# Performance work log

Measured on AMD Instinct MI355X. Metric: run time of the kernel, lower is better.

The kernel has to match this reference:

```python
import jax, jax.numpy as jnp
import numpy as np

B, S, D, H = 2, 2048, 1024, 16
DK = D // H


def setup_inputs() -> dict:
    key = jax.random.key(0)
    ks = jax.random.split(key, 12)
    sc = 1.0 / np.sqrt(D)
    inp = {
        "q": jax.random.normal(ks[0], (B, S, D), jnp.float32),
        "k": jax.random.normal(ks[1], (B, S, D), jnp.float32),
        "v": jax.random.normal(ks[2], (B, S, D), jnp.float32),
        # causal mask, broadcastable over batch and heads
        "mask": jnp.tril(jnp.ones((S, S), jnp.int32))[None, None],
        "Wq": jax.random.normal(ks[3], (D, D), jnp.float32) * sc,
        "bq": jax.random.normal(ks[4], (D,), jnp.float32) * 0.02,
        "Wk": jax.random.normal(ks[5], (D, D), jnp.float32) * sc,
        "bk": jax.random.normal(ks[6], (D,), jnp.float32) * 0.02,
        "Wv": jax.random.normal(ks[7], (D, D), jnp.float32) * sc,
        "bv": jax.random.normal(ks[8], (D,), jnp.float32) * 0.02,
        "Wo": jax.random.normal(ks[9], (D, D), jnp.float32) * sc,
        "bo": jax.random.normal(ks[10], (D,), jnp.float32) * 0.02,
    }
    return inp


def reference(q, k, v, mask, Wq, bq, Wk, bk, Wv, bv, Wo, bo):
    b, s, _ = q.shape
    # QKV projections (torch Linear: x @ W.T + b)
    qh = (q @ Wq.T + bq).reshape(b, s, H, DK).transpose(0, 2, 1, 3)  # [B,H,S,DK]
    kh = (k @ Wk.T + bk).reshape(b, -1, H, DK).transpose(0, 2, 1, 3)
    vh = (v @ Wv.T + bv).reshape(b, -1, H, DK).transpose(0, 2, 1, 3)
    scores = jnp.einsum("bhqd,bhkd->bhqk", qh, kh) / np.sqrt(DK)  # [B,H,S,S]
    scores = jnp.where(mask == 0, jnp.float32(-1e9), scores)
    attn = jax.nn.softmax(scores, axis=-1)
    # dropout p=0.0 (eval) -> identity
    x = jnp.einsum("bhqk,bhkd->bhqd", attn, vh)  # [B,H,S,DK]
    x = x.transpose(0, 2, 1, 3).reshape(b, s, H * DK)
    return x @ Wo.T + bo
```

## Files before the change

kernel.cpp:

```cpp
#include <hip/hip_runtime.h>
#include <hip/hip_bf16.h>
#include <cstdint>
#include <cstddef>

using u16   = unsigned short;
using u32   = uint32_t;
using u16x4 = __attribute__((ext_vector_type(4))) unsigned short;
using u16x8 = __attribute__((ext_vector_type(8))) unsigned short;
using s16x8 = __attribute__((ext_vector_type(8))) short;
using f32x4 = __attribute__((ext_vector_type(4))) float;
using f32x16 = __attribute__((ext_vector_type(16))) float;

#define B_DIM  2
#define S_DIM  2048
#define D_DIM  1024
#define H_DIM  16
#define DK_DIM 64

__device__ __forceinline__ u16 f2bf(float f) {
  union { float f; uint32_t u; } c; c.f = f;
  uint32_t u = c.u;
  return (u16)((u + 0x7FFFu + ((u >> 16) & 1u)) >> 16);
}
__device__ __forceinline__ float bf2f(u16 v) {
  union { uint32_t u; float f; } c; c.u = (uint32_t)v << 16;
  return c.f;
}

__device__ __forceinline__ void gload16(const void* g, void* l) {
  __builtin_amdgcn_global_load_lds(
      (const __attribute__((address_space(1))) void*)g,
      (__attribute__((address_space(3))) void*)l, 16, 0, 0);
}

__device__ __forceinline__ int chunk_base(int qt) {
  return (qt < 4) ? qt
       : (qt < 8) ? 4 + 2 * (qt - 4)
       : (qt < 12) ? 12 + 3 * (qt - 8)
       : 24 + 4 * (qt - 12);
}

__global__ __launch_bounds__(256) void cast_all_kernel(
    const float* q, const float* k, const float* v,
    const float* wq, const float* wk, const float* wv, const float* wo,
    u16* dq, u16* dk, u16* dv, u16* dwq, u16* dwk, u16* dwv, u16* dwo)
{
  const int f = blockIdx.x;
  const float* s; u16* d; int base;
  if (f < 6144) {
    int a = f >> 11;
    s = (a == 0) ? q : (a == 1) ? k : v;
    d = (a == 0) ? dq : (a == 1) ? dk : dv;
    base = (f & 2047) * 2048;
  } else {
    int a = (f - 6144) >> 9;
    s = (a == 0) ? wq : (a == 1) ? wk : (a == 2) ? wv : wo;
    d = (a == 0) ? dwq : (a == 1) ? dwk : (a == 2) ? dwv : dwo;
    base = ((f - 6144) & 511) * 2048;
  }
  int i = base + threadIdx.x * 8;
  f32x4 a = *(const f32x4*)(s + i);
  f32x4 b = *(const f32x4*)(s + i + 4);
  u16x8 ov;
  ov[0] = f2bf(a[0]); ov[1] = f2bf(a[1]); ov[2] = f2bf(a[2]); ov[3] = f2bf(a[3]);
  ov[4] = f2bf(b[0]); ov[5] = f2bf(b[1]); ov[6] = f2bf(b[2]); ov[7] = f2bf(b[3]);
  *(u16x8*)(d + i) = ov;
}

#define BM 128
#define BK 64

template <int BNT>
__device__ __forceinline__ void gemm_bt_core(
    const u16* __restrict__ A, const u16* __restrict__ W,
    const float* __restrict__ bias, void* __restrict__ out, int mode,
    int mtile, int ntile, float oscale)
{
  constexpr int NFRAG = BNT / 32;
  __shared__ u16 Alds[BM * BK];
  __shared__ u16 Blds[BNT * BK];
  const int K = 1024;
  const int tid = threadIdx.x;
  const int w = tid >> 6, l = tid & 63;
  const int lr = l & 15, lg = l >> 4;
  const int wr = w >> 1, wc = w & 1;
  const int m0 = mtile * BM, n0 = ntile * BNT;

  f32x4 acc[4][NFRAG] = {};

  for (int kt = 0; kt < K / BK; ++kt) {
    const int k0 = kt * BK;
    #pragma unroll
    for (int i = 0; i < 4; ++i) {
      int c = i * 256 + tid;
      int r = c >> 3;
      int cb = ((c & 7) << 4) ^ ((r & 7) << 4);
      gload16((const char*)(A + (size_t)(m0 + r) * K + k0) + cb,
              (char*)Alds + i * 4096 + w * 1024);
    }
    #pragma unroll
    for (int i = 0; i < BNT / 32; ++i) {
      int c = i * 256 + tid;
      int r = c >> 3;
      int cb = ((c & 7) << 4) ^ ((r & 7) << 4);
      gload16((const char*)(W + (size_t)(n0 + r) * K + k0) + cb,
              (char*)Blds + i * 4096 + w * 1024);
    }
    __syncthreads();
    #pragma unroll
    for (int ks = 0; ks < 2; ++ks) {
      s16x8 af[4], bf[NFRAG];
      #pragma unroll
      for (int mi = 0; mi < 4; ++mi) {
        int r = wr * 64 + mi * 16 + lr;
        int kb = (ks * 64 + lg * 16) ^ ((r & 7) << 4);
        af[mi] = *(const s16x8*)((const char*)Alds + r * 128 + kb);
      }
      #pragma unroll
      for (int ni = 0; ni < NFRAG; ++ni) {
        int r = wc * (BNT / 2) + ni * 16 + lr;
        int kb = (ks * 64 + lg * 16) ^ ((r & 7) << 4);
        bf[ni] = *(const s16x8*)((const char*)Blds + r * 128 + kb);
      }
      #pragma unroll
      for (int mi = 0; mi < 4; ++mi)
        #pragma unroll
        for (int ni = 0; ni < NFRAG; ++ni)
          acc[mi][ni] = __builtin_amdgcn_mfma_f32_16x16x32_bf16(
              af[mi], bf[ni], acc[mi][ni], 0, 0, 0);
    }
    __syncthreads();
  }

  const int mbase = m0 + wr * 64 + lg * 4;
  const int nbase = n0 + wc * (BNT / 2) + lr;
  #pragma unroll
  for (int ni = 0; ni < NFRAG; ++ni) {
    int n = nbase + ni * 16;
    float bb = bias[n];
    #pragma unroll
    for (int mi = 0; mi < 4; ++mi) {
      int mr = mbase + mi * 16;
      f32x4 vv = acc[mi][ni];
      if (mode == 2) {
        float* o = (float*)out;
        #pragma unroll
        for (int r = 0; r < 4; ++r) o[(size_t)(mr + r) * 1024 + n] = vv[r] + bb;
      } else if (mode == 0) {
        u16* o = (u16*)out;
        #pragma unroll
        for (int r = 0; r < 4; ++r)
          o[(size_t)(mr + r) * 1024 + n] = f2bf((vv[r] + bb) * oscale);
      } else if (mode == 3) {
        u16* o = (u16*)out;
        int h = n >> 6, d = n & 63;
        int db = d >> 4, hi8 = (d >> 3) & 1, e = d & 7;
        int bb_ = mr >> 11, j = mr & (S_DIM - 1);
        int jt = j >> 6, rh = (j >> 5) & 1, lq0 = j & 31;
        size_t base = (((size_t)(bb_ * H_DIM + h) * 32 + jt) * 8 + (db * 2 + rh))
                      * 512 + (size_t)(hi8 * 32) * 8 + e;
        #pragma unroll
        for (int r = 0; r < 4; ++r)
          o[base + (size_t)(lq0 + r) * 8] = f2bf(vv[r] + bb);
      } else {
        u16* o = (u16*)out;
        int h = n >> 6, dk = n & 63;
        int rh = dk >> 5, lq = dk & 31;
        int bb_ = mr >> 11, j = mr & (S_DIM - 1);
        int jt = j >> 6, jj = j & 63;
        int db = jj >> 4, hi8 = (jj >> 3) & 1, e0 = jj & 7;
        size_t base = (((size_t)(bb_ * H_DIM + h) * 32 + jt) * 8 + (db * 2 + rh))
                      * 512 + (size_t)(hi8 * 32 + lq) * 8 + e0;
        u16x4 pk;
        #pragma unroll
        for (int r = 0; r < 4; ++r) pk[r] = f2bf(vv[r] + bb);
        *(u16x4*)(o + base) = pk;
      }
    }
  }
}

__global__ __launch_bounds__(256, 5) void qkv_gemm_kernel(
    const u16* xq, const u16* xk, const u16* xv,
    const u16* wq, const u16* wk, const u16* wv,
    const float* bq, const float* bk, const float* bv,
    u16* qlin, u16* kfragb, u16* vfragb)
{
  const int f = blockIdx.x;
  const int xcd = f & 7;
  const int s = f >> 3;
  const int z = s >> 6;
  const int r = s & 63;
  const int mtile = xcd * 4 + (r >> 4);
  const int ntile = r & 15;

  const u16* A = (z == 0) ? xq : (z == 1) ? xk : xv;
  const u16* W = (z == 0) ? wq : (z == 1) ? wk : wv;
  const float* bias = (z == 0) ? bq : (z == 1) ? bk : bv;
  void* out = (z == 0) ? (void*)qlin : (z == 1) ? (void*)kfragb : (void*)vfragb;
  gemm_bt_core<64>(A, W, bias, out, (z == 0) ? 0 : (z == 1) ? 3 : 1, mtile, ntile,
                   (z == 0) ? 0.125f * 1.44269504f : 1.0f);
}

__global__ __launch_bounds__(256, 5) void oproj_kernel(
    const u16* aout, const u16* wo, const float* bo, float* out)
{
  const int f = blockIdx.x;
  const int xcd = f & 7;
  const int s = f >> 3;
  const int mtile = xcd * 4 + (s >> 5);
  const int ntile = s & 31;
  gemm_bt_core<32>(aout, wo, bo, (void*)out, 2, mtile, ntile, 1.0f);
}

__global__ __launch_bounds__(256, 3) void attn_kernel(
    const u16* __restrict__ qlin, const u16* __restrict__ kfrag,
    const u16* __restrict__ vfrag, u16* __restrict__ opart,
    float* __restrict__ lpart)
{
  const int tid = threadIdx.x;
  const int w = tid >> 6, l = tid & 63;
  const int lq = l & 31, hi = l >> 5;

  const int f = blockIdx.x;
  const int bh = f & 31;
  const int g = f >> 5;
  int qt, ch;
  if (g < 16)      { qt = 15 - (g >> 2);        ch = g & 3; }
  else if (g < 28) { qt = 11 - (g - 16) / 3;    ch = (g - 16) % 3; }
  else if (g < 36) { qt = 7 - ((g - 28) >> 1);  ch = (g - 28) & 1; }
  else             { qt = 3 - (g - 36);         ch = 0; }
  const int T  = 2 * qt + 2;
  const int nc = (T + 7) >> 3;
  const int jlo = (ch * T) / nc;
  const int jhi = ((ch + 1) * T) / nc;
  const int b = bh >> 4, h = bh & 15;

  const int qb  = qt * 128 + w * 32;
  const int myq = qb + lq;
  const int jtend_w = (qb + 31) >> 6;
  const int jend = (jhi < jtend_w + 1) ? jhi : (jtend_w + 1);

  s16x8 qf[4];
  {
    const u16* qptr = qlin + (size_t)(b * S_DIM + myq) * D_DIM + h * DK_DIM + hi * 8;
    #pragma unroll
    for (int db = 0; db < 4; ++db) qf[db] = *(const s16x8*)(qptr + db * 16);
  }

  f32x16 o0 = {}, o1 = {};
  float l_run = 0.f;

  const u16* kbase = kfrag + (size_t)bh * 32 * 4096;
  const u16* vbase = vfrag + (size_t)bh * 32 * 4096;

  s16x8 kf2[8], vf2[8];
  #pragma unroll
  for (int fk = 0; fk < 8; ++fk)
    kf2[fk] = *(const s16x8*)(kbase + (size_t)jlo * 4096 + fk * 512 + (size_t)l * 8);
  #pragma unroll
  for (int fk = 0; fk < 8; ++fk)
    vf2[fk] = *(const s16x8*)(vbase + (size_t)jlo * 4096 + fk * 512 + (size_t)l * 8);

  #pragma unroll 1
  for (int jt = jlo; jt < jend; ++jt) {
    const int j0 = jt * 64;

    f32x16 s0 = {}, s1 = {};
    #pragma unroll
    for (int db = 0; db < 4; ++db) {
      s0 = __builtin_amdgcn_mfma_f32_32x32x16_bf16(kf2[db * 2 + 0], qf[db], s0, 0, 0, 0);
      s1 = __builtin_amdgcn_mfma_f32_32x32x16_bf16(kf2[db * 2 + 1], qf[db], s1, 0, 0, 0);
    }

    if (jt + 1 < jend) {
      const u16* kbn = kbase + (size_t)(jt + 1) * 4096;
      #pragma unroll
      for (int fk = 0; fk < 8; ++fk)
        kf2[fk] = *(const s16x8*)(kbn + fk * 512 + (size_t)l * 8);
    }

    if (j0 + 63 > qb) {
      #pragma unroll
      for (int r = 0; r < 16; ++r) {
        int kr = (r & 3) + 8 * (r >> 2) + 4 * hi;
        if (j0 + kr > myq)      s0[r] = -1e30f;
        if (j0 + 32 + kr > myq) s1[r] = -1e30f;
      }
    }

    u32 wds[16];
    float ls = 0.f;
    #pragma unroll
    for (int i = 0; i < 8; ++i) {
      float pa = __builtin_amdgcn_exp2f(s0[2 * i]);
      float pb = __builtin_amdgcn_exp2f(s0[2 * i + 1]);
      ls += pa + pb;
      wds[i] = (u32)f2bf(pa) | ((u32)f2bf(pb) << 16);
      float pc = __builtin_amdgcn_exp2f(s1[2 * i]);
      float pd = __builtin_amdgcn_exp2f(s1[2 * i + 1]);
      ls += pc + pd;
      wds[8 + i] = (u32)f2bf(pc) | ((u32)f2bf(pd) << 16);
    }
    l_run += ls;

    #pragma unroll
    for (int ks = 0; ks < 4; ++ks) {
      u32 w0 = wds[4 * ks], w1 = wds[4 * ks + 1];
      u32 w2 = wds[4 * ks + 2], w3 = wds[4 * ks + 3];
      u32 ta = __shfl_xor(hi ? w0 : w2, 32);
      u32 tb = __shfl_xor(hi ? w1 : w3, 32);
      union { u32 u[4]; s16x8 v; } pf;
      pf.u[0] = hi ? ta : w0;
      pf.u[1] = hi ? tb : w1;
      pf.u[2] = hi ? w2 : ta;
      pf.u[3] = hi ? w3 : tb;
      o0 = __builtin_amdgcn_mfma_f32_32x32x16_bf16(vf2[ks * 2 + 0], pf.v, o0, 0, 0, 0);
      o1 = __builtin_amdgcn_mfma_f32_32x32x16_bf16(vf2[ks * 2 + 1], pf.v, o1, 0, 0, 0);
    }

    if (jt + 1 < jend) {
      const u16* vbn = vbase + (size_t)(jt + 1) * 4096;
      #pragma unroll
      for (int fk = 0; fk < 8; ++fk)
        vf2[fk] = *(const s16x8*)(vbn + fk * 512 + (size_t)l * 8);
    }
  }

  const size_t gslot = (size_t)bh * 40 + chunk_base(qt) + ch;
  u16* ob = opart + ((gslot * 128) + w * 32 + lq) * 64;
  #pragma unroll
  for (int rq = 0; rq < 4; ++rq) {
    u16x4 pk0, pk1;
    #pragma unroll
    for (int j = 0; j < 4; ++j) {
      pk0[j] = f2bf(o0[rq * 4 + j]);
      pk1[j] = f2bf(o1[rq * 4 + j]);
    }
    *(u16x4*)(ob + rq * 8 + hi * 4)      = pk0;
    *(u16x4*)(ob + 32 + rq * 8 + hi * 4) = pk1;
  }
  float lt = l_run + __shfl_xor(l_run, 32);
  if (hi == 0) lpart[gslot * 128 + w * 32 + lq] = lt;
}

__global__ __launch_bounds__(256) void attn_combine_kernel(
    const u16* __restrict__ opart, const float* __restrict__ lpart,
    u16* __restrict__ aout)
{
  const int f = blockIdx.x;
  const int bh = f & 31, qt = f >> 5;
  const int b = bh >> 4, h = bh & 15;
  const int nc = (2 * qt + 9) >> 3;
  const int cs = chunk_base(qt);

  const int t = threadIdx.x;
  const int row = t >> 1, dbase = (t & 1) * 32;
  float acc[32] = {};
  float lsum = 0.f;
  for (int c = 0; c < nc; ++c) {
    const size_t slot = (size_t)bh * 40 + cs + c;
    const u16* pr = opart + ((slot * 128) + row) * 64 + dbase;
    #pragma unroll
    for (int v4 = 0; v4 < 4; ++v4) {
      u16x8 vv = *(const u16x8*)(pr + v4 * 8);
      #pragma unroll
      for (int j = 0; j < 8; ++j) acc[v4 * 8 + j] += bf2f(vv[j]);
    }
    lsum += lpart[slot * 128 + row];
  }
  float inv = 1.f / lsum;
  u16* orow = aout + ((size_t)b * S_DIM + qt * 128 + row) * D_DIM + h * 64 + dbase;
  #pragma unroll
  for (int v4 = 0; v4 < 4; ++v4) {
    u16x8 ov;
    #pragma unroll
    for (int j = 0; j < 8; ++j) ov[j] = f2bf(acc[v4 * 8 + j] * inv);
    *(u16x8*)(orow + v4 * 8) = ov;
  }
}

extern "C" void kernel_launch(void* const* d_in, const int* in_sizes, int n_in,
                              void* d_out, int out_size, void* d_ws, size_t ws_size,
                              hipStream_t stream)
{
  (void)in_sizes; (void)n_in; (void)out_size; (void)ws_size;
  const float* q  = (const float*)d_in[0];
  const float* k  = (const float*)d_in[1];
  const float* v  = (const float*)d_in[2];
  const float* Wq = (const float*)d_in[4];
  const float* bq = (const float*)d_in[5];
  const float* Wk = (const float*)d_in[6];
  const float* bk = (const float*)d_in[7];
  const float* Wv = (const float*)d_in[8];
  const float* bv = (const float*)d_in[9];
  const float* Wo = (const float*)d_in[10];
  const float* bo = (const float*)d_in[11];
  float* out = (float*)d_out;

  const size_t XSZ = (size_t)B_DIM * S_DIM * D_DIM;
  const size_t WSZ = (size_t)D_DIM * D_DIM;

  u16* p = (u16*)d_ws;
  u16* qbf  = p; p += XSZ;
  u16* kbf  = p; p += XSZ;
  u16* vbf  = p; p += XSZ;
  u16* wqb  = p; p += WSZ;
  u16* wkb  = p; p += WSZ;
  u16* wvb  = p; p += WSZ;
  u16* wob  = p; p += WSZ;
  u16* qlin   = p; p += XSZ;
  u16* kfragb = p; p += XSZ;
  u16* vfragb = p; p += XSZ;
  u16* aoutb  = p; p += XSZ;

  u16*   opart = (u16*)d_ws;
  float* lpart = (float*)((char*)d_ws + (size_t)1280 * 128 * 64 * 2);

  cast_all_kernel<<<8192, 256, 0, stream>>>(
      q, k, v, Wq, Wk, Wv, Wo, qbf, kbf, vbf, wqb, wkb, wvb, wob);
  qkv_gemm_kernel<<<1536, 256, 0, stream>>>(
      qbf, kbf, vbf, wqb, wkb, wvb, bq, bk, bv, qlin, kfragb, vfragb);
  attn_kernel<<<1280, 256, 0, stream>>>(qlin, kfragb, vfragb, opart, lpart);
  attn_combine_kernel<<<512, 256, 0, stream>>>(opart, lpart, aoutb);
  oproj_kernel<<<1024, 256, 0, stream>>>(aoutb, wob, bo, out);
}
```

Measured before the change: 120.3 us.

## Use 256x256 double-buffered tiles in the QKV projection GEMM

The QKV GEMM changes from 128x64 tiles with 256 threads to 256x256 tiles with 512 threads, and shared-memory staging is double-buffered so the next K-slice loads while the current one computes. The goal is more data reuse per block and less barrier stall. The shared template is split apart, so the output projection now has its own specialized copy with the same tile sizes as before. The trade-off is only 192 blocks on the GPU, fewer than the CU count, so some CUs sit idle. Each block also uses much more LDS (128 KB) and more accumulator registers.

```diff
diff --git a/kernel.cpp b/kernel.cpp
--- a/kernel.cpp
+++ b/kernel.cpp
@@ -67,86 +67,103 @@
   *(u16x8*)(d + i) = ov;
 }
 
-#define BM 128
-#define BK 64
-
-template <int BNT>
-__device__ __forceinline__ void gemm_bt_core(
-    const u16* __restrict__ A, const u16* __restrict__ W,
-    const float* __restrict__ bias, void* __restrict__ out, int mode,
-    int mtile, int ntile, float oscale)
-{
-  constexpr int NFRAG = BNT / 32;
-  __shared__ u16 Alds[BM * BK];
-  __shared__ u16 Blds[BNT * BK];
+__global__ __launch_bounds__(512, 2) void qkv_gemm_kernel(
+    const u16* xq, const u16* xk, const u16* xv,
+    const u16* wq, const u16* wk, const u16* wv,
+    const float* bq, const float* bk, const float* bv,
+    u16* qlin, u16* kfragb, u16* vfragb)
+{
+  __shared__ u16 Alds[2][256 * 64];
+  __shared__ u16 Blds[2][256 * 64];
+  const int f = blockIdx.x;
+  const int xcd = f & 7;
+  const int s = f >> 3;
+  const int z = s >> 3;
+  const int r8 = s & 7;
+  const int mtile = xcd * 2 + (r8 >> 2);
+  const int ntile = r8 & 3;
+
+  const u16* A = (z == 0) ? xq : (z == 1) ? xk : xv;
+  const u16* W = (z == 0) ? wq : (z == 1) ? wk : wv;
+  const float* bias = (z == 0) ? bq : (z == 1) ? bk : bv;
+  void* out = (z == 0) ? (void*)qlin : (z == 1) ? (void*)kfragb : (void*)vfragb;
+  const int mode = (z == 0) ? 0 : (z == 1) ? 3 : 1;
+  const float oscale = (z == 0) ? 0.125f * 1.44269504f : 1.0f;
+
   const int K = 1024;
   const int tid = threadIdx.x;
   const int w = tid >> 6, l = tid & 63;
   const int lr = l & 15, lg = l >> 4;
-  const int wr = w >> 1, wc = w & 1;
-  const int m0 = mtile * BM, n0 = ntile * BNT;
-
-  f32x4 acc[4][NFRAG] = {};
-
-  for (int kt = 0; kt < K / BK; ++kt) {
-    const int k0 = kt * BK;
+  const int wm = w >> 2, wn = w & 3;
+  const int m0 = mtile * 256, n0 = ntile * 256;
+
+  f32x4 acc[8][4] = {};
+
+  auto stage = [&](int buf, int kt) {
+    const int k0 = kt * 64;
     #pragma unroll
     for (int i = 0; i < 4; ++i) {
-      int c = i * 256 + tid;
+      int c = i * 512 + tid;
       int r = c >> 3;
       int cb = ((c & 7) << 4) ^ ((r & 7) << 4);
       gload16((const char*)(A + (size_t)(m0 + r) * K + k0) + cb,
-              (char*)Alds + i * 4096 + w * 1024);
-    }
-    #pragma unroll
-    for (int i = 0; i < BNT / 32; ++i) {
-      int c = i * 256 + tid;
+              (char*)&Alds[buf][0] + i * 8192 + w * 1024);
+    }
+    #pragma unroll
+    for (int i = 0; i < 4; ++i) {
+      int c = i * 512 + tid;
       int r = c >> 3;
       int cb = ((c & 7) << 4) ^ ((r & 7) << 4);
       gload16((const char*)(W + (size_t)(n0 + r) * K + k0) + cb,
-              (char*)Blds + i * 4096 + w * 1024);
-    }
-    __syncthreads();
+              (char*)&Blds[buf][0] + i * 8192 + w * 1024);
+    }
+  };
+
+  stage(0, 0);
+
+  #pragma unroll 1
+  for (int kt = 0; kt < 16; ++kt) {
+    const int cur = kt & 1;
+    asm volatile("s_waitcnt vmcnt(0)" ::: "memory");
+    __builtin_amdgcn_s_barrier();
+    __builtin_amdgcn_sched_barrier(0);
+    if (kt + 1 < 16) stage(cur ^ 1, kt + 1);
+
     #pragma unroll
     for (int ks = 0; ks < 2; ++ks) {
-      s16x8 af[4], bf[NFRAG];
-      #pragma unroll
-      for (int mi = 0; mi < 4; ++mi) {
-        int r = wr * 64 + mi * 16 + lr;
+      s16x8 af[8], bf[4];
+      #pragma unroll
+      for (int mi = 0; mi < 8; ++mi) {
+        int r = wm * 128 + mi * 16 + lr;
         int kb = (ks * 64 + lg * 16) ^ ((r & 7) << 4);
-        af[mi] = *(const s16x8*)((const char*)Alds + r * 128 + kb);
-      }
-      #pragma unroll
-      for (int ni = 0; ni < NFRAG; ++ni) {
-        int r = wc * (BNT / 2) + ni * 16 + lr;
+        af[mi] = *(const s16x8*)((const char*)&Alds[cur][0] + r * 128 + kb);
+      }
+      #pragma unroll
+      for (int ni = 0; ni < 4; ++ni) {
+        int r = wn * 64 + ni * 16 + lr;
         int kb = (ks * 64 + lg * 16) ^ ((r & 7) << 4);
-        bf[ni] = *(const s16x8*)((const char*)Blds + r * 128 + kb);
-      }
-      #pragma unroll
-      for (int mi = 0; mi < 4; ++mi)
+        bf[ni] = *(const s16x8*)((const char*)&Blds[cur][0] + r * 128 + kb);
+      }
+      #pragma unroll
+      for (int mi = 0; mi < 8; ++mi)
         #pragma unroll
-        for (int ni = 0; ni < NFRAG; ++ni)
+        for (int ni = 0; ni < 4; ++ni)
           acc[mi][ni] = __builtin_amdgcn_mfma_f32_16x16x32_bf16(
               af[mi], bf[ni], acc[mi][ni], 0, 0, 0);
     }
-    __syncthreads();
-  }
-
-  const int mbase = m0 + wr * 64 + lg * 4;
-  const int nbase = n0 + wc * (BNT / 2) + lr;
+  }
+
+  const int mbase = m0 + wm * 128 + lg * 4;
+  const int nbase = n0 + wn * 64 + lr;
   #pragma unroll
-  for (int ni = 0; ni < NFRAG; ++ni) {
+  for (int ni = 0; ni < 4; ++ni) {
     int n = nbase + ni * 16;
     float bb = bias[n];
     #pragma unroll
-    for (int mi = 0; mi < 4; ++mi) {
+    for (int mi = 0; mi < 8; ++mi) {
       int mr = mbase + mi * 16;
       f32x4 vv = acc[mi][ni];
-      if (mode == 2) {
-        float* o = (float*)out;
-        #pragma unroll
-        for (int r = 0; r < 4; ++r) o[(size_t)(mr + r) * 1024 + n] = vv[r] + bb;
-      } else if (mode == 0) {
+      if (mode == 0) {
         u16* o = (u16*)out;
         #pragma unroll
         for (int r = 0; r < 4; ++r)
@@ -180,37 +197,84 @@
   }
 }
 
-__global__ __launch_bounds__(256, 5) void qkv_gemm_kernel(
-    const u16* xq, const u16* xk, const u16* xv,
-    const u16* wq, const u16* wk, const u16* wv,
-    const float* bq, const float* bk, const float* bv,
-    u16* qlin, u16* kfragb, u16* vfragb)
-{
-  const int f = blockIdx.x;
-  const int xcd = f & 7;
-  const int s = f >> 3;
-  const int z = s >> 6;
-  const int r = s & 63;
-  const int mtile = xcd * 4 + (r >> 4);
-  const int ntile = r & 15;
-
-  const u16* A = (z == 0) ? xq : (z == 1) ? xk : xv;
-  const u16* W = (z == 0) ? wq : (z == 1) ? wk : wv;
-  const float* bias = (z == 0) ? bq : (z == 1) ? bk : bv;
-  void* out = (z == 0) ? (void*)qlin : (z == 1) ? (void*)kfragb : (void*)vfragb;
-  gemm_bt_core<64>(A, W, bias, out, (z == 0) ? 0 : (z == 1) ? 3 : 1, mtile, ntile,
-                   (z == 0) ? 0.125f * 1.44269504f : 1.0f);
-}
+#define BM 128
+#define BK 64
 
 __global__ __launch_bounds__(256, 5) void oproj_kernel(
-    const u16* aout, const u16* wo, const float* bo, float* out)
-{
+    const u16* __restrict__ aout, const u16* __restrict__ wo,
+    const float* __restrict__ bo, float* __restrict__ out)
+{
+  constexpr int BNT = 32;
+  __shared__ u16 Alds[BM * BK];
+  __shared__ u16 Blds[BNT * BK];
   const int f = blockIdx.x;
   const int xcd = f & 7;
   const int s = f >> 3;
   const int mtile = xcd * 4 + (s >> 5);
   const int ntile = s & 31;
-  gemm_bt_core<32>(aout, wo, bo, (void*)out, 2, mtile, ntile, 1.0f);
+
+  const int K = 1024;
+  const int tid = threadIdx.x;
+  const int w = tid >> 6, l = tid & 63;
+  const int lr = l & 15, lg = l >> 4;
+  const int wr = w >> 1, wc = w & 1;
+  const int m0 = mtile * BM, n0 = ntile * BNT;
+
+  f32x4 acc[4][1] = {};
+
+  for (int kt = 0; kt < K / BK; ++kt) {
+    const int k0 = kt * BK;
+    #pragma unroll
+    for (int i = 0; i < 4; ++i) {
+      int c = i * 256 + tid;
+      int r = c >> 3;
+      int cb = ((c & 7) << 4) ^ ((r & 7) << 4);
+      gload16((const char*)(aout + (size_t)(m0 + r) * K + k0) + cb,
+              (char*)Alds + i * 4096 + w * 1024);
+    }
+    {
+      int c = tid;
+      int r = c >> 3;
+      int cb = ((c & 7) << 4) ^ ((r & 7) << 4);
+      gload16((const char*)(wo + (size_t)(n0 + r) * K + k0) + cb,
+              (char*)Blds + w * 1024);
+    }
+    __syncthreads();
+    #pragma unroll
+    for (int ks = 0; ks < 2; ++ks) {
+      s16x8 af[4], bf[1];
+      #pragma unroll
+      for (int mi = 0; mi < 4; ++mi) {
+        int r = wr * 64 + mi * 16 + lr;
+        int kb = (ks * 64 + lg * 16) ^ ((r & 7) << 4);
+        af[mi] = *(const s16x8*)((const char*)Alds + r * 128 + kb);
+      }
+      {
+        int r = wc * 16 + lr;
+        int kb = (ks * 64 + lg * 16) ^ ((r & 7) << 4);
+        bf[0] = *(const s16x8*)((const char*)Blds + r * 128 + kb);
+      }
+      #pragma unroll
+      for (int mi = 0; mi < 4; ++mi)
+        acc[mi][0] = __builtin_amdgcn_mfma_f32_16x16x32_bf16(
+            af[mi], bf[0], acc[mi][0], 0, 0, 0);
+    }
+    __syncthreads();
+  }
+
+  const int mbase = m0 + wr * 64 + lg * 4;
+  const int nbase = n0 + wc * 16 + lr;
+  {
+    int n = nbase;
+    float bb = bo[n];
+    #pragma unroll
+    for (int mi = 0; mi < 4; ++mi) {
+      int mr = mbase + mi * 16;
+      f32x4 vv = acc[mi][0];
+      #pragma unroll
+      for (int r = 0; r < 4; ++r) out[(size_t)(mr + r) * 1024 + n] = vv[r] + bb;
+    }
+  }
 }
 
 __global__ __launch_bounds__(256, 3) void attn_kernel(
@@ -419,7 +483,7 @@
 
   cast_all_kernel<<<8192, 256, 0, stream>>>(
       q, k, v, Wq, Wk, Wv, Wo, qbf, kbf, vbf, wqb, wkb, wvb, wob);
-  qkv_gemm_kernel<<<1536, 256, 0, stream>>>(
+  qkv_gemm_kernel<<<192, 512, 0, stream>>>(
       qbf, kbf, vbf, wqb, wkb, wvb, bq, bk, bv, qlin, kfragb, vfragb);
   attn_kernel<<<1280, 256, 0, stream>>>(qlin, kfragb, vfragb, opart, lpart);
   attn_combine_kernel<<<512, 256, 0, stream>>>(opart, lpart, aoutb);
```

Result: no change. 118.9 us (-1.1%).
